# Performance work log

Hardware: AMD Instinct MI355X
Metric: run time of the kernel (lower is better)

## Reference

```python
import jax, jax.numpy as jnp
import numpy as np

N = 20000
M = 32          # max_neighbors
IN_DIM = 256
OUT_DIM = 256
H = 4           # num_heads
D = OUT_DIM // H  # head_dim = 64
LN_EPS = 1e-5
NEG_INF = -1.0e9


def setup_inputs() -> dict:
    key = jax.random.key(0)
    ks = jax.random.split(key, 6)
    h = jax.random.normal(ks[0], (N, IN_DIM), dtype=jnp.float32)
    neighbor_idx = jax.random.randint(ks[1], (N, M), 0, N, dtype=jnp.int32)
    neighbor_mask = jax.random.randint(ks[2], (N, M), 0, 2, dtype=jnp.int32)
    # parameters (xavier-ish scaling)
    W = jax.random.normal(ks[3], (IN_DIM, OUT_DIM), dtype=jnp.float32) / np.sqrt(IN_DIM)
    a_l = jax.random.normal(ks[4], (H, D), dtype=jnp.float32) / np.sqrt(D)
    a_r = jax.random.normal(ks[5], (H, D), dtype=jnp.float32) / np.sqrt(D)
    ln_gamma = jnp.ones((OUT_DIM,), dtype=jnp.float32)
    ln_beta = jnp.zeros((OUT_DIM,), dtype=jnp.float32)
    return {"h": h, "neighbor_idx": neighbor_idx, "neighbor_mask": neighbor_mask,
            "W": W, "a_l": a_l, "a_r": a_r, "ln_gamma": ln_gamma, "ln_beta": ln_beta}


def reference(h, neighbor_idx, neighbor_mask, W, a_l, a_r, ln_gamma, ln_beta):
    h_proj = h @ W                                   # [N, OUT_DIM]
    h_heads = h_proj.reshape(N, H, D)                # [N, H, D]
    # per-node score halves; gathering scalars instead of full features for er
    el = jnp.einsum('nhd,hd->nh', h_heads, a_l)      # [N, H]
    er_node = jnp.einsum('nhd,hd->nh', h_heads, a_r) # [N, H]
    er = er_node[neighbor_idx]                       # [N, M, H]
    e = jax.nn.leaky_relu(el[:, None, :] + er, negative_slope=0.2)  # [N, M, H]
    e = jnp.where(neighbor_mask[:, :, None] == 0, NEG_INF, e)
    alpha = jax.nn.softmax(e, axis=1)                # softmax over neighbors
    neigh_h = h_heads[neighbor_idx]                  # [N, M, H, D]
    out_heads = jnp.einsum('nmh,nmhd->nhd', alpha, neigh_h)
    H_cat = out_heads.reshape(N, OUT_DIM)
    res = h_proj                                     # in_dim == out_dim -> res_proj is None
    out = jax.nn.gelu(H_cat + res, approximate=False)
    # LayerNorm over last dim
    mu = jnp.mean(out, axis=-1, keepdims=True)
    var = jnp.var(out, axis=-1, keepdims=True)
    out = (out - mu) * jax.lax.rsqrt(var + LN_EPS) * ln_gamma + ln_beta
    return out
```

## Files before the change

### kernel.cpp

```cpp
#include <hip/hip_runtime.h>
#include <math.h>

#define N_NODES 20000
#define M_NEI   32
#define DIM     256
#define H_HEADS 4
#define D_HEAD  64
#define LN_EPS  1e-5f
#define NEG_INF -1.0e9f
#define APAD    264

using short8  = __attribute__((ext_vector_type(8))) short;
using short4v = __attribute__((ext_vector_type(4))) short;
using floatx4 = __attribute__((ext_vector_type(4))) float;
using floatx2 = __attribute__((ext_vector_type(2))) float;
using uintx4  = __attribute__((ext_vector_type(4))) unsigned int;

__device__ __forceinline__ float bf2f(unsigned short u) {
    union { unsigned int i; float f; } c; c.i = ((unsigned int)u) << 16; return c.f;
}
__device__ __forceinline__ float u2f(unsigned int i) {
    union { unsigned int i; float f; } c; c.i = i; return c.f;
}
__device__ __forceinline__ unsigned short f2bf(float f) {
    union { float f; unsigned int i; } c; c.f = f;
    unsigned int x = c.i;
    x += 0x7fffu + ((x >> 16) & 1u);
    return (unsigned short)(x >> 16);
}
__device__ __forceinline__ bool in_is_fp32(const void* gamma) {
    return *(const unsigned int*)gamma == 0x3F800000u;
}

__global__ void k_prep(const void* __restrict__ W, const void* __restrict__ gamma,
                       unsigned short* __restrict__ Wt) {
    const bool f32 = in_is_fp32(gamma);
    const int n = blockIdx.x;
    const int k = threadIdx.x;
    float w = f32 ? ((const float*)W)[(size_t)k * DIM + n]
                  : bf2f(((const unsigned short*)W)[(size_t)k * DIM + n]);
    Wt[(size_t)n * DIM + k] = f2bf(w);
}

__global__ __launch_bounds__(256) void k_gemm(const void* __restrict__ A,
                                              const void* __restrict__ gamma,
                                              const unsigned short* __restrict__ Bt,
                                              const void* __restrict__ al,
                                              const void* __restrict__ ar,
                                              unsigned short* __restrict__ hp_h,
                                              float* __restrict__ el_h,
                                              float* __restrict__ er_h) {
    __shared__ unsigned short sA[32][APAD];
    const bool f32 = in_is_fp32(gamma);
    const int t    = threadIdx.x;
    const int m0   = blockIdx.x * 32;

    #pragma unroll
    for (int it = 0; it < 4; ++it) {
        int chunk = it * 256 + t;
        int row   = chunk >> 5;
        int c16   = chunk & 31;
        short8 v;
        if (!f32) {
            v = *(const short8*)((const unsigned short*)A + (size_t)(m0 + row) * DIM + c16 * 8);
        } else {
            const float* ap = (const float*)A + (size_t)(m0 + row) * DIM + c16 * 8;
            #pragma unroll
            for (int j = 0; j < 8; ++j) v[j] = (short)f2bf(ap[j]);
        }
        *(short8*)&sA[row][c16 * 8] = v;
    }
    __syncthreads();

    const int hd   = t >> 6;
    const int lane = t & 63;
    const int r    = lane & 15;
    const int quad = lane >> 4;
    const int n0   = hd * 64;

    floatx4 acc[2][4];
    #pragma unroll
    for (int rf = 0; rf < 2; ++rf)
        #pragma unroll
        for (int c = 0; c < 4; ++c) acc[rf][c] = (floatx4){0.f, 0.f, 0.f, 0.f};

    #pragma unroll
    for (int k0 = 0; k0 < DIM; k0 += 32) {
        short8 a0 = *(const short8*)&sA[r][k0 + quad * 8];
        short8 a1 = *(const short8*)&sA[16 + r][k0 + quad * 8];
        #pragma unroll
        for (int c = 0; c < 4; ++c) {
            short8 b = *(const short8*)(Bt + (size_t)(n0 + c * 16 + r) * DIM + k0 + quad * 8);
            acc[0][c] = __builtin_amdgcn_mfma_f32_16x16x32_bf16(a0, b, acc[0][c], 0, 0, 0);
            acc[1][c] = __builtin_amdgcn_mfma_f32_16x16x32_bf16(a1, b, acc[1][c], 0, 0, 0);
        }
    }

    float alv[4], arv[4];
    #pragma unroll
    for (int c = 0; c < 4; ++c) {
        int col = n0 + c * 16 + r;
        if (f32) { alv[c] = ((const float*)al)[col]; arv[c] = ((const float*)ar)[col]; }
        else     { alv[c] = bf2f(((const unsigned short*)al)[col]);
                   arv[c] = bf2f(((const unsigned short*)ar)[col]); }
    }

    #pragma unroll
    for (int rf = 0; rf < 2; ++rf) {
        #pragma unroll
        for (int rr = 0; rr < 4; ++rr) {
            const int row = m0 + rf * 16 + quad * 4 + rr;
            float sl = 0.f, sr = 0.f;
            #pragma unroll
            for (int c = 0; c < 4; ++c) {
                float v = acc[rf][c][rr];
                sl += v * alv[c];
                sr += v * arv[c];
                hp_h[((size_t)hd * N_NODES + row) * D_HEAD + c * 16 + r] = f2bf(v);
            }
            #pragma unroll
            for (int off = 1; off < 16; off <<= 1) {
                sl += __shfl_xor(sl, off);
                sr += __shfl_xor(sr, off);
            }
            if (r == 0) {
                el_h[(size_t)hd * N_NODES + row] = sl;
                er_h[(size_t)hd * N_NODES + row] = sr;
            }
        }
    }
}

__global__ __launch_bounds__(256) void k_attn_h(const int* __restrict__ nidx,
                                                const int* __restrict__ nmask,
                                                const unsigned short* __restrict__ hp_h,
                                                const float* __restrict__ el_h,
                                                const float* __restrict__ er_h,
                                                unsigned short* __restrict__ out_h) {
    __shared__ int2 s_oa[32][33];

    const int hd  = blockIdx.x & 3;
    const int nb0 = (blockIdx.x >> 2) * 32;
    const int t   = threadIdx.x;

    {
        const int m   = t & 31;
        const int sub = t >> 5;
        #pragma unroll
        for (int it = 0; it < 4; ++it) {
            const int nl  = it * 8 + sub;
            const int n   = nb0 + nl;
            const int idx = nidx[(size_t)n * M_NEI + m];
            const int msk = nmask[(size_t)n * M_NEI + m];
            float e = el_h[(size_t)hd * N_NODES + n] + er_h[(size_t)hd * N_NODES + idx];
            e = (e > 0.f) ? e : 0.2f * e;
            e = msk ? e : NEG_INF;
            float mx = e;
            #pragma unroll
            for (int off = 1; off < 32; off <<= 1) mx = fmaxf(mx, __shfl_xor(mx, off, 32));
            float a = expf(e - mx);
            float sm = a;
            #pragma unroll
            for (int off = 1; off < 32; off <<= 1) sm += __shfl_xor(sm, off, 32);
            int2 oa;
            oa.x = idx * (D_HEAD * 2);
            union { float f; int i; } c; c.f = a / sm;
            oa.y = c.i;
            s_oa[nl][m] = oa;
        }
    }
    __syncthreads();

    const int wave = t >> 6;
    const int lane = t & 63;
    const int g    = lane >> 3;
    const int s    = lane & 7;
    const int nl   = wave * 8 + g;
    const int n    = nb0 + nl;
    const char* tbl = (const char*)hp_h + (size_t)hd * N_NODES * (D_HEAD * 2) + s * 16;

    floatx2 acc[4];
    #pragma unroll
    for (int j = 0; j < 4; ++j) acc[j] = (floatx2){0.f, 0.f};

    #pragma unroll
    for (int m = 0; m < M_NEI; ++m) {
        const int2  oa = s_oa[nl][m];
        const float aa = u2f((unsigned int)oa.y);
        uintx4 u = *(const uintx4*)(tbl + oa.x);
        #pragma unroll
        for (int j = 0; j < 4; ++j) {
            floatx2 f = { u2f(u[j] << 16), u2f(u[j] & 0xffff0000u) };
            acc[j] += (floatx2){aa, aa} * f;
        }
    }

    {
        uintx4 u = *(const uintx4*)((const char*)hp_h
                     + ((size_t)hd * N_NODES + n) * (D_HEAD * 2) + s * 16);
        #pragma unroll
        for (int j = 0; j < 4; ++j) {
            floatx2 f = { u2f(u[j] << 16), u2f(u[j] & 0xffff0000u) };
            acc[j] += f;
        }
    }

    short8 o;
    #pragma unroll
    for (int j = 0; j < 4; ++j) {
        o[2 * j]     = (short)f2bf(acc[j][0]);
        o[2 * j + 1] = (short)f2bf(acc[j][1]);
    }
    *(short8*)(out_h + ((size_t)hd * N_NODES + n) * D_HEAD + s * 8) = o;
}

__global__ __launch_bounds__(256) void k_final(const unsigned short* __restrict__ out_h,
                                               const void* __restrict__ gamma,
                                               const void* __restrict__ beta,
                                               void* __restrict__ out) {
    const bool f32 = in_is_fp32(gamma);
    const int wave = threadIdx.x >> 6;
    const int lane = threadIdx.x & 63;
    const int n    = blockIdx.x * 4 + wave;
    const int h    = lane >> 4;
    const int d0   = (lane & 15) * 4;

    const size_t off = ((size_t)h * N_NODES + n) * D_HEAD + d0;
    short4v ov = *(const short4v*)(out_h + off);

    float x[4], s1 = 0.f, s2 = 0.f;
    #pragma unroll
    for (int i = 0; i < 4; ++i) {
        float xi = bf2f((unsigned short)ov[i]);
        xi = 0.5f * xi * (1.f + erff(xi * 0.70710678118654752f));
        x[i] = xi;
        s1 += xi;
        s2 += xi * xi;
    }
    #pragma unroll
    for (int offv = 1; offv < 64; offv <<= 1) {
        s1 += __shfl_xor(s1, offv);
        s2 += __shfl_xor(s2, offv);
    }
    const float mu  = s1 * (1.f / 256.f);
    float var = s2 * (1.f / 256.f) - mu * mu;
    var = fmaxf(var, 0.f);
    const float inv = rsqrtf(var + LN_EPS);

    if (f32) {
        const float* gp = (const float*)gamma + lane * 4;
        const float* bp = (const float*)beta  + lane * 4;
        float* op = (float*)out + (size_t)n * DIM + lane * 4;
        #pragma unroll
        for (int i = 0; i < 4; ++i)
            op[i] = (x[i] - mu) * inv * gp[i] + bp[i];
    } else {
        const unsigned short* gp = (const unsigned short*)gamma + lane * 4;
        const unsigned short* bp = (const unsigned short*)beta  + lane * 4;
        short4v o;
        #pragma unroll
        for (int i = 0; i < 4; ++i) {
            float y = (x[i] - mu) * inv * bf2f(gp[i]) + bf2f(bp[i]);
            o[i] = (short)f2bf(y);
        }
        *(short4v*)((unsigned short*)out + (size_t)n * DIM + lane * 4) = o;
    }
}

extern "C" void kernel_launch(void* const* d_in, const int* in_sizes, int n_in,
                              void* d_out, int out_size, void* d_ws, size_t ws_size,
                              hipStream_t stream) {
    const void* h     = d_in[0];
    const int*  nidx  = (const int*)d_in[1];
    const int*  nmask = (const int*)d_in[2];
    const void* W     = d_in[3];
    const void* al    = d_in[4];
    const void* ar    = d_in[5];
    const void* gamma = d_in[6];
    const void* beta  = d_in[7];

    unsigned short* Wt    = (unsigned short*)d_ws;
    unsigned short* hp_h  = (unsigned short*)((char*)d_ws + 131072);
    unsigned short* out_h = (unsigned short*)((char*)d_ws + 10371072);
    float* el_h = (float*)((char*)d_ws + 20611072);
    float* er_h = (float*)((char*)d_ws + 20931072);

    k_prep<<<DIM, 256, 0, stream>>>(W, gamma, Wt);
    k_gemm<<<N_NODES / 32, 256, 0, stream>>>(h, gamma, Wt, al, ar, hp_h, el_h, er_h);
    k_attn_h<<<H_HEADS * (N_NODES / 32), 256, 0, stream>>>(nidx, nmask, hp_h, el_h, er_h, out_h);
    k_final<<<N_NODES / 4, 256, 0, stream>>>(out_h, gamma, beta, d_out);
}
```

Before: 135.9 us.

## Merge four kernels into two persistent kernels with software grid barriers

Folds the weight transpose into the projection kernel and the attention and LayerNorm stages into one kernel, both run as persistent grids sized from occupancy, with atomic-based grid barriers in place of kernel boundaries. This removes two launches and the gaps between them. In exchange it adds spin-wait barriers, serialises on the slowest block, and relies on every block being co-resident, which could deadlock if occupancy is misestimated. The W transpose is also now spread across blocks via a grid-stride loop.

```diff
diff --git a/kernel.cpp b/kernel.cpp
--- a/kernel.cpp
+++ b/kernel.cpp
@@ -32,69 +32,53 @@
     return *(const unsigned int*)gamma == 0x3F800000u;
 }
 
-__global__ void k_prep(const void* __restrict__ W, const void* __restrict__ gamma,
-                       unsigned short* __restrict__ Wt) {
-    const bool f32 = in_is_fp32(gamma);
-    const int n = blockIdx.x;
-    const int k = threadIdx.x;
-    float w = f32 ? ((const float*)W)[(size_t)k * DIM + n]
-                  : bf2f(((const unsigned short*)W)[(size_t)k * DIM + n]);
-    Wt[(size_t)n * DIM + k] = f2bf(w);
-}
-
-__global__ __launch_bounds__(256) void k_gemm(const void* __restrict__ A,
+__device__ int g_cnt1 = 0, g_gen1 = 0, g_cnt2 = 0, g_gen2 = 0;
+
+__device__ __forceinline__ void grid_bar(int* cnt, int* gen, int nb) {
+    __syncthreads();
+    if (threadIdx.x == 0) {
+        __threadfence();
+        int g = __hip_atomic_load(gen, __ATOMIC_RELAXED, __HIP_MEMORY_SCOPE_AGENT);
+        if (__hip_atomic_fetch_add(cnt, 1, __ATOMIC_ACQ_REL, __HIP_MEMORY_SCOPE_AGENT) == nb - 1) {
+            __hip_atomic_store(cnt, 0, __ATOMIC_RELAXED, __HIP_MEMORY_SCOPE_AGENT);
+            __hip_atomic_store(gen, g + 1, __ATOMIC_RELEASE, __HIP_MEMORY_SCOPE_AGENT);
+        } else {
+            while (__hip_atomic_load(gen, __ATOMIC_ACQUIRE, __HIP_MEMORY_SCOPE_AGENT) == g)
+                __builtin_amdgcn_s_sleep(2);
+        }
+        __threadfence();
+    }
+    __syncthreads();
+}
+
+__global__ __launch_bounds__(256) void k_proj(const void* __restrict__ A,
+                                              const void* __restrict__ W,
                                               const void* __restrict__ gamma,
-                                              const unsigned short* __restrict__ Bt,
                                               const void* __restrict__ al,
                                               const void* __restrict__ ar,
+                                              unsigned short* __restrict__ Wt,
                                               unsigned short* __restrict__ hp_h,
                                               float* __restrict__ el_h,
-                                              float* __restrict__ er_h) {
+                                              float* __restrict__ er_h,
+                                              int G1) {
     __shared__ unsigned short sA[32][APAD];
     const bool f32 = in_is_fp32(gamma);
-    const int t    = threadIdx.x;
-    const int m0   = blockIdx.x * 32;
-
-    #pragma unroll
-    for (int it = 0; it < 4; ++it) {
-        int chunk = it * 256 + t;
-        int row   = chunk >> 5;
-        int c16   = chunk & 31;
-        short8 v;
-        if (!f32) {
-            v = *(const short8*)((const unsigned short*)A + (size_t)(m0 + row) * DIM + c16 * 8);
-        } else {
-            const float* ap = (const float*)A + (size_t)(m0 + row) * DIM + c16 * 8;
-            #pragma unroll
-            for (int j = 0; j < 8; ++j) v[j] = (short)f2bf(ap[j]);
-        }
-        *(short8*)&sA[row][c16 * 8] = v;
-    }
-    __syncthreads();
+    const int  b   = blockIdx.x;
+    const int  t   = threadIdx.x;
+
+    for (int idx = b * 256 + t; idx < DIM * DIM; idx += G1 * 256) {
+        const int n = idx >> 8, k = idx & 255;
+        float w = f32 ? ((const float*)W)[(size_t)k * DIM + n]
+                      : bf2f(((const unsigned short*)W)[(size_t)k * DIM + n]);
+        Wt[idx] = f2bf(w);
+    }
+    grid_bar(&g_cnt1, &g_gen1, G1);
 
     const int hd   = t >> 6;
     const int lane = t & 63;
     const int r    = lane & 15;
     const int quad = lane >> 4;
     const int n0   = hd * 64;
-
-    floatx4 acc[2][4];
-    #pragma unroll
-    for (int rf = 0; rf < 2; ++rf)
-        #pragma unroll
-        for (int c = 0; c < 4; ++c) acc[rf][c] = (floatx4){0.f, 0.f, 0.f, 0.f};
-
-    #pragma unroll
-    for (int k0 = 0; k0 < DIM; k0 += 32) {
-        short8 a0 = *(const short8*)&sA[r][k0 + quad * 8];
-        short8 a1 = *(const short8*)&sA[16 + r][k0 + quad * 8];
-        #pragma unroll
-        for (int c = 0; c < 4; ++c) {
-            short8 b = *(const short8*)(Bt + (size_t)(n0 + c * 16 + r) * DIM + k0 + quad * 8);
-            acc[0][c] = __builtin_amdgcn_mfma_f32_16x16x32_bf16(a0, b, acc[0][c], 0, 0, 0);
-            acc[1][c] = __builtin_amdgcn_mfma_f32_16x16x32_bf16(a1, b, acc[1][c], 0, 0, 0);
-        }
-    }
 
     float alv[4], arv[4];
     #pragma unroll
@@ -105,165 +89,214 @@
                    arv[c] = bf2f(((const unsigned short*)ar)[col]); }
     }
 
-    #pragma unroll
-    for (int rf = 0; rf < 2; ++rf) {
-        #pragma unroll
-        for (int rr = 0; rr < 4; ++rr) {
-            const int row = m0 + rf * 16 + quad * 4 + rr;
-            float sl = 0.f, sr = 0.f;
+    for (int tile = b; tile < N_NODES / 32; tile += G1) {
+        const int m0 = tile * 32;
+
+        #pragma unroll
+        for (int it = 0; it < 4; ++it) {
+            int chunk = it * 256 + t;
+            int row   = chunk >> 5;
+            int c16   = chunk & 31;
+            short8 v;
+            if (!f32) {
+                v = *(const short8*)((const unsigned short*)A + (size_t)(m0 + row) * DIM + c16 * 8);
+            } else {
+                const float* ap = (const float*)A + (size_t)(m0 + row) * DIM + c16 * 8;
+                #pragma unroll
+                for (int j = 0; j < 8; ++j) v[j] = (short)f2bf(ap[j]);
+            }
+            *(short8*)&sA[row][c16 * 8] = v;
+        }
+        __syncthreads();
+
+        floatx4 acc[2][4];
+        #pragma unroll
+        for (int rf = 0; rf < 2; ++rf)
+            #pragma unroll
+            for (int c = 0; c < 4; ++c) acc[rf][c] = (floatx4){0.f, 0.f, 0.f, 0.f};
+
+        #pragma unroll
+        for (int k0 = 0; k0 < DIM; k0 += 32) {
+            short8 a0 = *(const short8*)&sA[r][k0 + quad * 8];
+            short8 a1 = *(const short8*)&sA[16 + r][k0 + quad * 8];
             #pragma unroll
             for (int c = 0; c < 4; ++c) {
-                float v = acc[rf][c][rr];
-                sl += v * alv[c];
-                sr += v * arv[c];
-                hp_h[((size_t)hd * N_NODES + row) * D_HEAD + c * 16 + r] = f2bf(v);
-            }
-            #pragma unroll
-            for (int off = 1; off < 16; off <<= 1) {
-                sl += __shfl_xor(sl, off);
-                sr += __shfl_xor(sr, off);
-            }
-            if (r == 0) {
-                el_h[(size_t)hd * N_NODES + row] = sl;
-                er_h[(size_t)hd * N_NODES + row] = sr;
-            }
-        }
-    }
-}
-
-__global__ __launch_bounds__(256) void k_attn_h(const int* __restrict__ nidx,
-                                                const int* __restrict__ nmask,
-                                                const unsigned short* __restrict__ hp_h,
-                                                const float* __restrict__ el_h,
-                                                const float* __restrict__ er_h,
-                                                unsigned short* __restrict__ out_h) {
+                short8 bfr = *(const short8*)(Wt + (size_t)(n0 + c * 16 + r) * DIM + k0 + quad * 8);
+                acc[0][c] = __builtin_amdgcn_mfma_f32_16x16x32_bf16(a0, bfr, acc[0][c], 0, 0, 0);
+                acc[1][c] = __builtin_amdgcn_mfma_f32_16x16x32_bf16(a1, bfr, acc[1][c], 0, 0, 0);
+            }
+        }
+
+        #pragma unroll
+        for (int rf = 0; rf < 2; ++rf) {
+            #pragma unroll
+            for (int rr = 0; rr < 4; ++rr) {
+                const int row = m0 + rf * 16 + quad * 4 + rr;
+                float sl = 0.f, sr = 0.f;
+                #pragma unroll
+                for (int c = 0; c < 4; ++c) {
+                    float v = acc[rf][c][rr];
+                    sl += v * alv[c];
+                    sr += v * arv[c];
+                    hp_h[((size_t)hd * N_NODES + row) * D_HEAD + c * 16 + r] = f2bf(v);
+                }
+                #pragma unroll
+                for (int off = 1; off < 16; off <<= 1) {
+                    sl += __shfl_xor(sl, off);
+                    sr += __shfl_xor(sr, off);
+                }
+                if (r == 0) {
+                    el_h[(size_t)hd * N_NODES + row] = sl;
+                    er_h[(size_t)hd * N_NODES + row] = sr;
+                }
+            }
+        }
+        __syncthreads();
+    }
+}
+
+__global__ __launch_bounds__(256) void k_attn_final(const int* __restrict__ nidx,
+                                                    const int* __restrict__ nmask,
+                                                    const unsigned short* __restrict__ hp_h,
+                                                    const float* __restrict__ el_h,
+                                                    const float* __restrict__ er_h,
+                                                    const void* __restrict__ gamma,
+                                                    const void* __restrict__ beta,
+                                                    unsigned short* __restrict__ out_h,
+                                                    void* __restrict__ out,
+                                                    int G2) {
     __shared__ int2 s_oa[32][33];
 
-    const int hd  = blockIdx.x & 3;
-    const int nb0 = (blockIdx.x >> 2) * 32;
-    const int t   = threadIdx.x;
-
-    {
-        const int m   = t & 31;
-        const int sub = t >> 5;
-        #pragma unroll
-        for (int it = 0; it < 4; ++it) {
-            const int nl  = it * 8 + sub;
-            const int n   = nb0 + nl;
-            const int idx = nidx[(size_t)n * M_NEI + m];
-            const int msk = nmask[(size_t)n * M_NEI + m];
-            float e = el_h[(size_t)hd * N_NODES + n] + er_h[(size_t)hd * N_NODES + idx];
-            e = (e > 0.f) ? e : 0.2f * e;
-            e = msk ? e : NEG_INF;
-            float mx = e;
-            #pragma unroll
-            for (int off = 1; off < 32; off <<= 1) mx = fmaxf(mx, __shfl_xor(mx, off, 32));
-            float a = expf(e - mx);
-            float sm = a;
-            #pragma unroll
-            for (int off = 1; off < 32; off <<= 1) sm += __shfl_xor(sm, off, 32);
-            int2 oa;
-            oa.x = idx * (D_HEAD * 2);
-            union { float f; int i; } c; c.f = a / sm;
-            oa.y = c.i;
-            s_oa[nl][m] = oa;
-        }
-    }
-    __syncthreads();
-
+    const int b    = blockIdx.x;
+    const int t    = threadIdx.x;
     const int wave = t >> 6;
     const int lane = t & 63;
-    const int g    = lane >> 3;
-    const int s    = lane & 7;
-    const int nl   = wave * 8 + g;
-    const int n    = nb0 + nl;
-    const char* tbl = (const char*)hp_h + (size_t)hd * N_NODES * (D_HEAD * 2) + s * 16;
-
-    floatx2 acc[4];
-    #pragma unroll
-    for (int j = 0; j < 4; ++j) acc[j] = (floatx2){0.f, 0.f};
-
-    #pragma unroll
-    for (int m = 0; m < M_NEI; ++m) {
-        const int2  oa = s_oa[nl][m];
-        const float aa = u2f((unsigned int)oa.y);
-        uintx4 u = *(const uintx4*)(tbl + oa.x);
-        #pragma unroll
-        for (int j = 0; j < 4; ++j) {
-            floatx2 f = { u2f(u[j] << 16), u2f(u[j] & 0xffff0000u) };
-            acc[j] += (floatx2){aa, aa} * f;
-        }
-    }
-
-    {
-        uintx4 u = *(const uintx4*)((const char*)hp_h
-                     + ((size_t)hd * N_NODES + n) * (D_HEAD * 2) + s * 16);
-        #pragma unroll
-        for (int j = 0; j < 4; ++j) {
-            floatx2 f = { u2f(u[j] << 16), u2f(u[j] & 0xffff0000u) };
-            acc[j] += f;
-        }
-    }
-
-    short8 o;
-    #pragma unroll
-    for (int j = 0; j < 4; ++j) {
-        o[2 * j]     = (short)f2bf(acc[j][0]);
-        o[2 * j + 1] = (short)f2bf(acc[j][1]);
-    }
-    *(short8*)(out_h + ((size_t)hd * N_NODES + n) * D_HEAD + s * 8) = o;
-}
-
-__global__ __launch_bounds__(256) void k_final(const unsigned short* __restrict__ out_h,
-                                               const void* __restrict__ gamma,
-                                               const void* __restrict__ beta,
-                                               void* __restrict__ out) {
+
+    for (int u = b; u < H_HEADS * (N_NODES / 32); u += G2) {
+        const int hd  = u & 3;
+        const int nb0 = (u >> 2) * 32;
+
+        {
+            const int m   = t & 31;
+            const int sub = t >> 5;
+            #pragma unroll
+            for (int it = 0; it < 4; ++it) {
+                const int nl  = it * 8 + sub;
+                const int n   = nb0 + nl;
+                const int idx = nidx[(size_t)n * M_NEI + m];
+                const int msk = nmask[(size_t)n * M_NEI + m];
+                float e = el_h[(size_t)hd * N_NODES + n] + er_h[(size_t)hd * N_NODES + idx];
+                e = (e > 0.f) ? e : 0.2f * e;
+                e = msk ? e : NEG_INF;
+                float mx = e;
+                #pragma unroll
+                for (int off = 1; off < 32; off <<= 1) mx = fmaxf(mx, __shfl_xor(mx, off, 32));
+                float a = expf(e - mx);
+                float sm = a;
+                #pragma unroll
+                for (int off = 1; off < 32; off <<= 1) sm += __shfl_xor(sm, off, 32);
+                int2 oa;
+                oa.x = idx * (D_HEAD * 2);
+                union { float f; int i; } c; c.f = a / sm;
+                oa.y = c.i;
+                s_oa[nl][m] = oa;
+            }
+        }
+        __syncthreads();
+
+        {
+            const int g  = lane >> 3;
+            const int s  = lane & 7;
+            const int nl = wave * 8 + g;
+            const int n  = nb0 + nl;
+            const char* tbl = (const char*)hp_h + (size_t)hd * N_NODES * (D_HEAD * 2) + s * 16;
+
+            floatx2 acc[4];
+            #pragma unroll
+            for (int j = 0; j < 4; ++j) acc[j] = (floatx2){0.f, 0.f};
+
+            #pragma unroll
+            for (int m = 0; m < M_NEI; ++m) {
+                const int2  oa = s_oa[nl][m];
+                const float aa = u2f((unsigned int)oa.y);
+                uintx4 uu = *(const uintx4*)(tbl + oa.x);
+                #pragma unroll
+                for (int j = 0; j < 4; ++j) {
+                    floatx2 f = { u2f(uu[j] << 16), u2f(uu[j] & 0xffff0000u) };
+                    acc[j] += (floatx2){aa, aa} * f;
+                }
+            }
+
+            {
+                uintx4 uu = *(const uintx4*)((const char*)hp_h
+                             + ((size_t)hd * N_NODES + n) * (D_HEAD * 2) + s * 16);
+                #pragma unroll
+                for (int j = 0; j < 4; ++j) {
+                    floatx2 f = { u2f(uu[j] << 16), u2f(uu[j] & 0xffff0000u) };
+                    acc[j] += f;
+                }
+            }
+
+            short8 o;
+            #pragma unroll
+            for (int j = 0; j < 4; ++j) {
+                o[2 * j]     = (short)f2bf(acc[j][0]);
+                o[2 * j + 1] = (short)f2bf(acc[j][1]);
+            }
+            *(short8*)(out_h + ((size_t)hd * N_NODES + n) * D_HEAD + s * 8) = o;
+        }
+        __syncthreads();
+    }
+
+    grid_bar(&g_cnt2, &g_gen2, G2);
+
     const bool f32 = in_is_fp32(gamma);
-    const int wave = threadIdx.x >> 6;
-    const int lane = threadIdx.x & 63;
-    const int n    = blockIdx.x * 4 + wave;
-    const int h    = lane >> 4;
-    const int d0   = (lane & 15) * 4;
-
-    const size_t off = ((size_t)h * N_NODES + n) * D_HEAD + d0;
-    short4v ov = *(const short4v*)(out_h + off);
-
-    float x[4], s1 = 0.f, s2 = 0.f;
-    #pragma unroll
-    for (int i = 0; i < 4; ++i) {
-        float xi = bf2f((unsigned short)ov[i]);
-        xi = 0.5f * xi * (1.f + erff(xi * 0.70710678118654752f));
-        x[i] = xi;
-        s1 += xi;
-        s2 += xi * xi;
-    }
-    #pragma unroll
-    for (int offv = 1; offv < 64; offv <<= 1) {
-        s1 += __shfl_xor(s1, offv);
-        s2 += __shfl_xor(s2, offv);
-    }
-    const float mu  = s1 * (1.f / 256.f);
-    float var = s2 * (1.f / 256.f) - mu * mu;
-    var = fmaxf(var, 0.f);
-    const float inv = rsqrtf(var + LN_EPS);
-
-    if (f32) {
-        const float* gp = (const float*)gamma + lane * 4;
-        const float* bp = (const float*)beta  + lane * 4;
-        float* op = (float*)out + (size_t)n * DIM + lane * 4;
-        #pragma unroll
-        for (int i = 0; i < 4; ++i)
-            op[i] = (x[i] - mu) * inv * gp[i] + bp[i];
-    } else {
-        const unsigned short* gp = (const unsigned short*)gamma + lane * 4;
-        const unsigned short* bp = (const unsigned short*)beta  + lane * 4;
-        short4v o;
+    const int  fh  = lane >> 4;
+    const int  fd0 = (lane & 15) * 4;
+
+    for (int u = b; u < N_NODES / 4; u += G2) {
+        const int n = u * 4 + wave;
+
+        const size_t off = ((size_t)fh * N_NODES + n) * D_HEAD + fd0;
+        short4v ov = *(const short4v*)(out_h + off);
+
+        float x[4], s1 = 0.f, s2 = 0.f;
         #pragma unroll
         for (int i = 0; i < 4; ++i) {
-            float y = (x[i] - mu) * inv * bf2f(gp[i]) + bf2f(bp[i]);
-            o[i] = (short)f2bf(y);
-        }
-        *(short4v*)((unsigned short*)out + (size_t)n * DIM + lane * 4) = o;
+            float xi = bf2f((unsigned short)ov[i]);
+            xi = 0.5f * xi * (1.f + erff(xi * 0.70710678118654752f));
+            x[i] = xi;
+            s1 += xi;
+            s2 += xi * xi;
+        }
+        #pragma unroll
+        for (int offv = 1; offv < 64; offv <<= 1) {
+            s1 += __shfl_xor(s1, offv);
+            s2 += __shfl_xor(s2, offv);
+        }
+        const float mu  = s1 * (1.f / 256.f);
+        float var = s2 * (1.f / 256.f) - mu * mu;
+        var = fmaxf(var, 0.f);
+        const float inv = rsqrtf(var + LN_EPS);
+
+        if (f32) {
+            const float* gp = (const float*)gamma + lane * 4;
+            const float* bp = (const float*)beta  + lane * 4;
+            float* op = (float*)out + (size_t)n * DIM + lane * 4;
+            #pragma unroll
+            for (int i = 0; i < 4; ++i)
+                op[i] = (x[i] - mu) * inv * gp[i] + bp[i];
+        } else {
+            const unsigned short* gp = (const unsigned short*)gamma + lane * 4;
+            const unsigned short* bp = (const unsigned short*)beta  + lane * 4;
+            short4v o;
+            #pragma unroll
+            for (int i = 0; i < 4; ++i) {
+                float y = (x[i] - mu) * inv * bf2f(gp[i]) + bf2f(bp[i]);
+                o[i] = (short)f2bf(y);
+            }
+            *(short4v*)((unsigned short*)out + (size_t)n * DIM + lane * 4) = o;
+        }
     }
 }
 
@@ -285,8 +318,21 @@
     float* el_h = (float*)((char*)d_ws + 20611072);
     float* er_h = (float*)((char*)d_ws + 20931072);
 
-    k_prep<<<DIM, 256, 0, stream>>>(W, gamma, Wt);
-    k_gemm<<<N_NODES / 32, 256, 0, stream>>>(h, gamma, Wt, al, ar, hp_h, el_h, er_h);
-    k_attn_h<<<H_HEADS * (N_NODES / 32), 256, 0, stream>>>(nidx, nmask, hp_h, el_h, er_h, out_h);
-    k_final<<<N_NODES / 4, 256, 0, stream>>>(out_h, gamma, beta, d_out);
-}
+    static int g1 = 0, g2 = 0;
+    if (g1 == 0) {
+        int b1 = 0, b2 = 0;
+        hipOccupancyMaxActiveBlocksPerMultiprocessor(&b1, k_proj, 256, 0);
+        hipOccupancyMaxActiveBlocksPerMultiprocessor(&b2, k_attn_final, 256, 0);
+        if (b1 < 1) b1 = 1;
+        if (b2 < 1) b2 = 1;
+        int cap1 = b1 * 256;
+        int cap2 = (b2 * 256) & ~7;
+        g1 = cap1 < (N_NODES / 32) ? cap1 : (N_NODES / 32);
+        g2 = cap2 < 2496 ? cap2 : 2496;
+        if (g2 < 8) g2 = 8;
+    }
+
+    k_proj<<<g1, 256, 0, stream>>>(h, W, gamma, al, ar, Wt, hp_h, el_h, er_h, g1);
+    k_attn_final<<<g2, 256, 0, stream>>>(nidx, nmask, hp_h, el_h, er_h, gamma, beta,
+                                         out_h, d_out, g2);
+}
```

After: 500.9 us. 269% more time.

## Fuse weight transpose into GEMM by loading W directly into registers

Applied to the files above, without the earlier changes.

Drops the separate k_prep kernel that transposed and converted W to bf16. Each GEMM wave now loads its B fragments straight from the original row-major W into registers before the main loop, and launch bounds are set for two blocks per CU. This removes one kernel launch and the round trip through the transposed weight buffer. In exchange, every block re-reads W with strided scalar loads and holds 128 extra registers of B fragments, which may limit occupancy.

```diff
diff --git a/kernel.cpp b/kernel.cpp
--- a/kernel.cpp
+++ b/kernel.cpp
@@ -32,28 +32,48 @@
     return *(const unsigned int*)gamma == 0x3F800000u;
 }
 
-__global__ void k_prep(const void* __restrict__ W, const void* __restrict__ gamma,
-                       unsigned short* __restrict__ Wt) {
-    const bool f32 = in_is_fp32(gamma);
-    const int n = blockIdx.x;
-    const int k = threadIdx.x;
-    float w = f32 ? ((const float*)W)[(size_t)k * DIM + n]
-                  : bf2f(((const unsigned short*)W)[(size_t)k * DIM + n]);
-    Wt[(size_t)n * DIM + k] = f2bf(w);
-}
-
-__global__ __launch_bounds__(256) void k_gemm(const void* __restrict__ A,
-                                              const void* __restrict__ gamma,
-                                              const unsigned short* __restrict__ Bt,
-                                              const void* __restrict__ al,
-                                              const void* __restrict__ ar,
-                                              unsigned short* __restrict__ hp_h,
-                                              float* __restrict__ el_h,
-                                              float* __restrict__ er_h) {
+__global__ __launch_bounds__(256, 2) void k_gemm(const void* __restrict__ A,
+                                                 const void* __restrict__ gamma,
+                                                 const void* __restrict__ W,
+                                                 const void* __restrict__ al,
+                                                 const void* __restrict__ ar,
+                                                 unsigned short* __restrict__ hp_h,
+                                                 float* __restrict__ el_h,
+                                                 float* __restrict__ er_h) {
     __shared__ unsigned short sA[32][APAD];
     const bool f32 = in_is_fp32(gamma);
     const int t    = threadIdx.x;
     const int m0   = blockIdx.x * 32;
+    const int hd   = t >> 6;
+    const int lane = t & 63;
+    const int r    = lane & 15;
+    const int quad = lane >> 4;
+    const int n0   = hd * 64;
+
+    short8 breg[4][8];
+    if (f32) {
+        #pragma unroll
+        for (int c = 0; c < 4; ++c) {
+            const float* wp = (const float*)W + (size_t)quad * 8 * DIM + n0 + c * 16 + r;
+            #pragma unroll
+            for (int kq = 0; kq < 8; ++kq) {
+                #pragma unroll
+                for (int j = 0; j < 8; ++j)
+                    breg[c][kq][j] = (short)f2bf(wp[(size_t)(kq * 32 + j) * DIM]);
+            }
+        }
+    } else {
+        #pragma unroll
+        for (int c = 0; c < 4; ++c) {
+            const unsigned short* wp = (const unsigned short*)W + (size_t)quad * 8 * DIM + n0 + c * 16 + r;
+            #pragma unroll
+            for (int kq = 0; kq < 8; ++kq) {
+                #pragma unroll
+                for (int j = 0; j < 8; ++j)
+                    breg[c][kq][j] = (short)wp[(size_t)(kq * 32 + j) * DIM];
+            }
+        }
+    }
 
     #pragma unroll
     for (int it = 0; it < 4; ++it) {
@@ -72,12 +92,6 @@
     }
     __syncthreads();
 
-    const int hd   = t >> 6;
-    const int lane = t & 63;
-    const int r    = lane & 15;
-    const int quad = lane >> 4;
-    const int n0   = hd * 64;
-
     floatx4 acc[2][4];
     #pragma unroll
     for (int rf = 0; rf < 2; ++rf)
@@ -85,14 +99,13 @@
         for (int c = 0; c < 4; ++c) acc[rf][c] = (floatx4){0.f, 0.f, 0.f, 0.f};
 
     #pragma unroll
-    for (int k0 = 0; k0 < DIM; k0 += 32) {
-        short8 a0 = *(const short8*)&sA[r][k0 + quad * 8];
-        short8 a1 = *(const short8*)&sA[16 + r][k0 + quad * 8];
+    for (int kq = 0; kq < 8; ++kq) {
+        short8 a0 = *(const short8*)&sA[r][kq * 32 + quad * 8];
+        short8 a1 = *(const short8*)&sA[16 + r][kq * 32 + quad * 8];
         #pragma unroll
         for (int c = 0; c < 4; ++c) {
-            short8 b = *(const short8*)(Bt + (size_t)(n0 + c * 16 + r) * DIM + k0 + quad * 8);
-            acc[0][c] = __builtin_amdgcn_mfma_f32_16x16x32_bf16(a0, b, acc[0][c], 0, 0, 0);
-            acc[1][c] = __builtin_amdgcn_mfma_f32_16x16x32_bf16(a1, b, acc[1][c], 0, 0, 0);
+            acc[0][c] = __builtin_amdgcn_mfma_f32_16x16x32_bf16(a0, breg[c][kq], acc[0][c], 0, 0, 0);
+            acc[1][c] = __builtin_amdgcn_mfma_f32_16x16x32_bf16(a1, breg[c][kq], acc[1][c], 0, 0, 0);
         }
     }
 
@@ -279,14 +292,12 @@
     const void* gamma = d_in[6];
     const void* beta  = d_in[7];
 
-    unsigned short* Wt    = (unsigned short*)d_ws;
     unsigned short* hp_h  = (unsigned short*)((char*)d_ws + 131072);
     unsigned short* out_h = (unsigned short*)((char*)d_ws + 10371072);
     float* el_h = (float*)((char*)d_ws + 20611072);
     float* er_h = (float*)((char*)d_ws + 20931072);
 
-    k_prep<<<DIM, 256, 0, stream>>>(W, gamma, Wt);
-    k_gemm<<<N_NODES / 32, 256, 0, stream>>>(h, gamma, Wt, al, ar, hp_h, el_h, er_h);
+    k_gemm<<<N_NODES / 32, 256, 0, stream>>>(h, gamma, W, al, ar, hp_h, el_h, er_h);
     k_attn_h<<<H_HEADS * (N_NODES / 32), 256, 0, stream>>>(nidx, nmask, hp_h, el_h, er_h, out_h);
     k_final<<<N_NODES / 4, 256, 0, stream>>>(out_h, gamma, beta, d_out);
 }
```

Result: no change. 133.7 us (-1.7%).
